# Kernel tuning notes

Measured on AMD Instinct MI355X. Metric: run time of the kernel, lower is better.

The kernel has to match this reference:

```python
import jax, jax.numpy as jnp
import numpy as np

UNITS = 256
LB = -17.0
UB = 8.0
STEP = 0.05
NUM_BUCKETS = int((UB - LB) / STEP) + 1  # 501
RESIDUE = LB - STEP
W_INIT = 0.5
BATCH = 65536


def setup_inputs() -> dict:
    key = jax.random.key(0)
    kx, = jax.random.split(key, 1)
    x = jax.random.normal(kx, (BATCH, UNITS), dtype=jnp.float32)
    v = jnp.ones((UNITS, NUM_BUCKETS), dtype=jnp.float32) * W_INIT
    b = jnp.zeros((UNITS,), dtype=jnp.float32)
    return {"x": x, "v": v, "b": b}


def reference(x, v, b):
    # x: (batch, units); v: (units, num_buckets); b: (units,)
    x_clipped = jnp.clip(x, LB + 1e-9, UB - 1e-9)
    indx = ((x_clipped - LB + STEP) / STEP).astype(jnp.int32)
    indx = jnp.clip(indx, 0, NUM_BUCKETS - 1)  # (batch, units)
    delta = x_clipped - LB + STEP - indx.astype(x.dtype) * STEP

    w = jax.nn.relu(v)  # (units, num_buckets)
    # exclusive cumsum over buckets: csum[u, j] = sum_{k<j} w[u, k]
    csum = jnp.cumsum(w, axis=1)
    csum = jnp.concatenate([jnp.zeros((w.shape[0], 1), w.dtype), csum[:, :-1]], axis=1)

    unit_idx = jnp.arange(UNITS)[None, :]  # (1, units) broadcasts with indx
    csum_g = csum[unit_idx, indx]  # (batch, units)
    w_g = w[unit_idx, indx]        # (batch, units)

    # Equivalent to sum over buckets of (triangular step mask + scattered delta) * relu(v)
    logits = STEP * csum_g + delta * w_g + RESIDUE + b[None, :]
    return jax.nn.sigmoid(logits)
```

## Files before the change

kernel.cpp:

```cpp
#include <hip/hip_runtime.h>

#define UNITS 256
#define NB 501
#define UPB 16
#define BT 1024
#define THREADS 512
#define STEPF 0.05f
#define LBF -17.0f
#define UBF 8.0f
#define RESIDUEF -17.05f

__global__ __launch_bounds__(THREADS, 4) void iso_fused_kernel(
    const float* __restrict__ x, const float* __restrict__ v,
    const float* __restrict__ bias, float* __restrict__ out, int nbb) {
  __shared__ float2 tab[UPB * NB];

  const int bu = blockIdx.x & (UNITS / UPB - 1);
  const int bb = blockIdx.x >> 4;
  const int u0 = bu * UPB;

  const int wave = threadIdx.x >> 6;
  const int lane = threadIdx.x & 63;
#pragma unroll
  for (int s = 0; s < 2; ++s) {
    const int ul = wave * 2 + s;
    const int u = u0 + ul;
    const float* vu = v + u * NB;
    float w[8], pref[8];
    float run = 0.0f;
#pragma unroll
    for (int k = 0; k < 8; ++k) {
      const int j = lane * 8 + k;
      const float wv = (j < NB) ? fmaxf(vu[j], 0.0f) : 0.0f;
      w[k] = wv;
      pref[k] = run;
      run += wv;
    }
    float s_inc = run;
#pragma unroll
    for (int d = 1; d < 64; d <<= 1) {
      const float o = __shfl_up(s_inc, d, 64);
      if (lane >= d) s_inc += o;
    }
    const float base = s_inc - run;
    const float off = RESIDUEF + bias[u];
#pragma unroll
    for (int k = 0; k < 8; ++k) {
      const int j = lane * 8 + k;
      if (j < NB)
        tab[ul * NB + j] = make_float2(STEPF * (base + pref[k]) + off, w[k]);
    }
  }
  __syncthreads();

  const int r = threadIdx.x >> 2;
  const int q = threadIdx.x & 3;
  const float4* __restrict__ x4 = reinterpret_cast<const float4*>(x);
  float4* __restrict__ o4 = reinterpret_cast<float4*>(out);
  const int row0 = bb * BT;

#pragma unroll
  for (int p = 0; p < BT / 128; ++p) {
    const int row = row0 + p * 128 + r;
    const int g = row * (UNITS / 4) + (u0 >> 2) + q;
    const float4 xv = x4[g];
    const float xs[4] = {xv.x, xv.y, xv.z, xv.w};
    float os[4];
#pragma unroll
    for (int k = 0; k < 4; ++k) {
      const float xc = fminf(fmaxf(xs[k], LBF + 1e-9f), UBF - 1e-9f);
      const float t = xc - LBF + STEPF;
      int idx = (int)(t * 20.0f);
      idx = idx < 0 ? 0 : (idx > NB - 1 ? NB - 1 : idx);
      const float delta = t - (float)idx * STEPF;
      const float2 cw = tab[(4 * q + k) * NB + idx];
      const float logit = cw.x + delta * cw.y;
      os[k] = 1.0f / (1.0f + __expf(-logit));
    }
    o4[g] = make_float4(os[0], os[1], os[2], os[3]);
  }
}

extern "C" void kernel_launch(void* const* d_in, const int* in_sizes, int n_in,
                              void* d_out, int out_size, void* d_ws,
                              size_t ws_size, hipStream_t stream) {
  const float* x = (const float*)d_in[0];
  const float* v = (const float*)d_in[1];
  const float* b = (const float*)d_in[2];
  float* out = (float*)d_out;

  const int rows = out_size / UNITS;
  const int nbb = rows / BT;
  const int grid = (UNITS / UPB) * nbb;
  iso_fused_kernel<<<grid, THREADS, 0, stream>>>(x, v, b, out, nbb);
}
```

Baseline: 148.1 us.

## Precompute lookup table in separate kernel and cache only hot window in LDS

Moves the per-unit relu/cumsum table build into a small preceding kernel that writes a global table to workspace, so each main block no longer recomputes the scan for its 16 units. The main kernel loads only a 256-entry window of buckets around the dense region of the input distribution into LDS, shrinking shared memory to allow 8 blocks per CU, and falls back to global reads for indices outside the window. The table constant is folded so the logit becomes a single fma of t. The price is an extra kernel launch, a workspace round trip, and divergent global loads for outliers. The window choice is tuned to normally distributed inputs but stays correct for any input.

```diff
diff --git a/kernel.cpp b/kernel.cpp
--- a/kernel.cpp
+++ b/kernel.cpp
@@ -2,54 +2,68 @@
 
 #define UNITS 256
 #define NB 501
-#define UPB 16
-#define BT 1024
-#define THREADS 512
 #define STEPF 0.05f
 #define LBF -17.0f
 #define UBF 8.0f
 #define RESIDUEF -17.05f
 
-__global__ __launch_bounds__(THREADS, 4) void iso_fused_kernel(
-    const float* __restrict__ x, const float* __restrict__ v,
-    const float* __restrict__ bias, float* __restrict__ out, int nbb) {
-  __shared__ float2 tab[UPB * NB];
+#define WLO 192
+#define WSZ 256
+#define UPB 16
+#define THREADS 512
+#define ROWS_PB 1024
+
+__global__ __launch_bounds__(256) void build_table_kernel(
+    const float* __restrict__ v, const float* __restrict__ b,
+    float2* __restrict__ gtab) {
+  const int lane = threadIdx.x & 63;
+  const int wave = threadIdx.x >> 6;
+  const int u = blockIdx.x * 4 + wave;
+  if (u >= UNITS) return;
+
+  const float* vu = v + u * NB;
+  float w[8], pref[8];
+  float run = 0.0f;
+#pragma unroll
+  for (int k = 0; k < 8; ++k) {
+    const int j = lane * 8 + k;
+    const float wv = (j < NB) ? fmaxf(vu[j], 0.0f) : 0.0f;
+    w[k] = wv;
+    pref[k] = run;
+    run += wv;
+  }
+  float s = run;
+#pragma unroll
+  for (int d = 1; d < 64; d <<= 1) {
+    const float o = __shfl_up(s, d, 64);
+    if (lane >= d) s += o;
+  }
+  const float base = s - run;
+  const float off = RESIDUEF + b[u];
+#pragma unroll
+  for (int k = 0; k < 8; ++k) {
+    const int j = lane * 8 + k;
+    if (j < NB) {
+      const float C = STEPF * (base + pref[k]) + off - (float)j * STEPF * w[k];
+      gtab[u * NB + j] = make_float2(C, w[k]);
+    }
+  }
+}
+
+__global__ __launch_bounds__(THREADS, 8) void iso_main_kernel(
+    const float* __restrict__ x, const float2* __restrict__ gtab,
+    float* __restrict__ out) {
+  __shared__ float2 tab[UPB * WSZ];
 
   const int bu = blockIdx.x & (UNITS / UPB - 1);
   const int bb = blockIdx.x >> 4;
   const int u0 = bu * UPB;
 
-  const int wave = threadIdx.x >> 6;
-  const int lane = threadIdx.x & 63;
 #pragma unroll
-  for (int s = 0; s < 2; ++s) {
-    const int ul = wave * 2 + s;
-    const int u = u0 + ul;
-    const float* vu = v + u * NB;
-    float w[8], pref[8];
-    float run = 0.0f;
-#pragma unroll
-    for (int k = 0; k < 8; ++k) {
-      const int j = lane * 8 + k;
-      const float wv = (j < NB) ? fmaxf(vu[j], 0.0f) : 0.0f;
-      w[k] = wv;
-      pref[k] = run;
-      run += wv;
-    }
-    float s_inc = run;
-#pragma unroll
-    for (int d = 1; d < 64; d <<= 1) {
-      const float o = __shfl_up(s_inc, d, 64);
-      if (lane >= d) s_inc += o;
-    }
-    const float base = s_inc - run;
-    const float off = RESIDUEF + bias[u];
-#pragma unroll
-    for (int k = 0; k < 8; ++k) {
-      const int j = lane * 8 + k;
-      if (j < NB)
-        tab[ul * NB + j] = make_float2(STEPF * (base + pref[k]) + off, w[k]);
-    }
+  for (int i = threadIdx.x; i < UPB * WSZ; i += THREADS) {
+    const int ul = i >> 8;
+    const int j = i & (WSZ - 1);
+    tab[i] = gtab[(u0 + ul) * NB + WLO + j];
   }
   __syncthreads();
 
@@ -57,10 +71,10 @@
   const int q = threadIdx.x & 3;
   const float4* __restrict__ x4 = reinterpret_cast<const float4*>(x);
   float4* __restrict__ o4 = reinterpret_cast<float4*>(out);
-  const int row0 = bb * BT;
+  const int row0 = bb * ROWS_PB;
 
-#pragma unroll
-  for (int p = 0; p < BT / 128; ++p) {
+#pragma unroll 4
+  for (int p = 0; p < ROWS_PB / 128; ++p) {
     const int row = row0 + p * 128 + r;
     const int g = row * (UNITS / 4) + (u0 >> 2) + q;
     const float4 xv = x4[g];
@@ -72,9 +86,15 @@
       const float t = xc - LBF + STEPF;
       int idx = (int)(t * 20.0f);
       idx = idx < 0 ? 0 : (idx > NB - 1 ? NB - 1 : idx);
-      const float delta = t - (float)idx * STEPF;
-      const float2 cw = tab[(4 * q + k) * NB + idx];
-      const float logit = cw.x + delta * cw.y;
+      const int ul = 4 * q + k;
+      const unsigned iw = (unsigned)(idx - WLO);
+      float2 cw;
+      if (iw < WSZ) {
+        cw = tab[ul * WSZ + (int)iw];
+      } else {
+        cw = gtab[(u0 + ul) * NB + idx];
+      }
+      const float logit = fmaf(t, cw.y, cw.x);
       os[k] = 1.0f / (1.0f + __expf(-logit));
     }
     o4[g] = make_float4(os[0], os[1], os[2], os[3]);
@@ -88,9 +108,11 @@
   const float* v = (const float*)d_in[1];
   const float* b = (const float*)d_in[2];
   float* out = (float*)d_out;
+  float2* gtab = (float2*)d_ws;
+
+  build_table_kernel<<<64, 256, 0, stream>>>(v, b, gtab);
 
   const int rows = out_size / UNITS;
-  const int nbb = rows / BT;
-  const int grid = (UNITS / UPB) * nbb;
-  iso_fused_kernel<<<grid, THREADS, 0, stream>>>(x, v, b, out, nbb);
+  const int grid = (UNITS / UPB) * (rows / ROWS_PB);
+  iso_main_kernel<<<grid, THREADS, 0, stream>>>(x, gtab, out);
 }
```

Measured after the change: 142.8 us. 1.04x faster.
